# Performance work log

Hardware: AMD Instinct MI355X
Metric: run time of the kernel (lower is better)

Reference implementation:

```python
import jax, jax.numpy as jnp
import numpy as np

INPUT_DIM = 128
HIDDEN = 64
NUM_LAYERS = 2
BATCH = 1024
SEQ = 512


def setup_inputs() -> dict:
    key = jax.random.key(0)
    ks = jax.random.split(key, 1 + 4 * NUM_LAYERS + 2)
    inp = {"x": jax.random.normal(ks[0], (BATCH, SEQ, INPUT_DIM), dtype=jnp.float32)}
    # PyTorch LSTM params per layer: W_ih [4H, in], W_hh [4H, H], b_ih [4H], b_hh [4H]
    # gate order: i, f, g, o. Init scale ~ 1/sqrt(H) like PyTorch uniform init.
    s = 1.0 / np.sqrt(HIDDEN)
    ki = 1
    for l in range(NUM_LAYERS):
        in_dim = INPUT_DIM if l == 0 else HIDDEN
        inp[f"W_ih{l}"] = jax.random.uniform(ks[ki], (4 * HIDDEN, in_dim), jnp.float32, -s, s); ki += 1
        inp[f"W_hh{l}"] = jax.random.uniform(ks[ki], (4 * HIDDEN, HIDDEN), jnp.float32, -s, s); ki += 1
        inp[f"b_ih{l}"] = jax.random.uniform(ks[ki], (4 * HIDDEN,), jnp.float32, -s, s); ki += 1
        inp[f"b_hh{l}"] = jax.random.uniform(ks[ki], (4 * HIDDEN,), jnp.float32, -s, s); ki += 1
    inp["fc_w"] = jax.random.uniform(ks[ki], (1, HIDDEN), jnp.float32, -s, s); ki += 1
    inp["fc_b"] = jax.random.uniform(ks[ki], (1,), jnp.float32, -s, s)
    return inp


def _lstm_layer(x, W_ih, W_hh, b_ih, b_hh):
    # x: [B, T, in] -> h_seq: [B, T, H]
    B, T, _ = x.shape
    H = W_hh.shape[1]
    # Precompute input contribution for all timesteps (the big GEMM).
    xg = jnp.einsum('bti,gi->btg', x, W_ih) + b_ih + b_hh  # [B, T, 4H]

    def step(carry, xg_t):
        h, c = carry
        g = xg_t + h @ W_hh.T  # [B, 4H]
        i, f, gg, o = jnp.split(g, 4, axis=-1)
        i = jax.nn.sigmoid(i)
        f = jax.nn.sigmoid(f)
        gg = jnp.tanh(gg)
        o = jax.nn.sigmoid(o)
        c = f * c + i * gg
        h = o * jnp.tanh(c)
        return (h, c), h

    init = (jnp.zeros((B, H), x.dtype), jnp.zeros((B, H), x.dtype))
    _, hs = jax.lax.scan(step, init, jnp.swapaxes(xg, 0, 1))  # hs: [T, B, H]
    return jnp.swapaxes(hs, 0, 1)


def reference(x, W_ih0, W_hh0, b_ih0, b_hh0, W_ih1, W_hh1, b_ih1, b_hh1, fc_w, fc_b):
    h = _lstm_layer(x, W_ih0, W_hh0, b_ih0, b_hh0)
    h = _lstm_layer(h, W_ih1, W_hh1, b_ih1, b_hh1)  # dropout inactive at inference
    last = h[:, -1, :]  # [B, H]
    return jax.nn.sigmoid(last @ fc_w.T + fc_b)  # [B, 1]
```

## Files before the change

kernel.cpp:

```cpp
#include <hip/hip_runtime.h>
#include <hip/hip_bf16.h>

using short8  = __attribute__((ext_vector_type(8))) short;
using float4v = __attribute__((ext_vector_type(4))) float;
using uint2v  = __attribute__((ext_vector_type(2))) unsigned int;
using u32 = unsigned int;
using u16 = unsigned short;

#define MFMA(a,b,cc) __builtin_amdgcn_mfma_f32_16x16x32_bf16((a),(b),(cc),0,0,0)
#define PIPE_BARRIER() asm volatile("s_waitcnt lgkmcnt(0)\n\ts_barrier" ::: "memory")
#define LOG2E 1.44269504088896340736f

static __device__ __forceinline__ float fexp2(float x){ return __builtin_amdgcn_exp2f(x); }
static __device__ __forceinline__ float frcp(float x){ return __builtin_amdgcn_rcpf(x); }

static __device__ __forceinline__ short f2bf(float f){
  __hip_bfloat16 h = __float2bfloat16(f);
  return __builtin_bit_cast(short, h);
}
static __device__ __forceinline__ short8 load_bf8s(const float* p, float s){
  short8 v;
#pragma unroll
  for (int j = 0; j < 8; ++j) v[j] = f2bf(p[j] * s);
  return v;
}
static __device__ __forceinline__ float bflo(u32 d){ return __builtin_bit_cast(float, d << 16); }
static __device__ __forceinline__ float bfhi(u32 d){ return __builtin_bit_cast(float, d & 0xffff0000u); }

static __device__ __forceinline__ float gates1(float ai, float af, float ag, float ao, float& cst){
  float iv = frcp(1.f + fexp2(ai));
  float fv = frcp(1.f + fexp2(af));
  float ov = frcp(1.f + fexp2(ao));
  float gv = 1.f - 2.f * frcp(1.f + fexp2(ag));
  float cn = fv * cst + iv * gv;
  cst = cn;
  float tc = 1.f - 2.f * frcp(1.f + fexp2((2.f*LOG2E) * cn));
  return ov * tc;
}

template<int KK>
static __device__ __forceinline__ void gm4_part(int t0, const float* xlane,
    float4v (&xr)[4][2], float4v (&acc)[4], const short8 (&wA)[4][4])
{
  short8 xb;
#pragma unroll
  for (int j = 0; j < 4; ++j){ xb[j] = f2bf(xr[KK][0][j]); xb[4+j] = f2bf(xr[KK][1][j]); }
  int tn = t0 + 4; if (tn > 508) tn = 508;
  const float* nx = xlane + (size_t)tn * 128 + KK*32;
  xr[KK][0] = *(const float4v*)nx;
  xr[KK][1] = *(const float4v*)(nx + 4);
  acc[0] = MFMA(xb, wA[0][KK], acc[0]);
  acc[1] = MFMA(xb, wA[1][KK], acc[1]);
  acc[2] = MFMA(xb, wA[2][KK], acc[2]);
  acc[3] = MFMA(xb, wA[3][KK], acc[3]);
}

static __device__ __forceinline__ void gm4_store(int t0,
    float4v (&acc)[4], u32 (&xgb)[8][4][132], int c, int kg, int wl)
{
  u32* base = &xgb[(t0 + kg) & 7][0][(wl*16 + c)*2];
#pragma unroll
  for (int r = 0; r < 4; ++r){
    u32 d0 = (u32)(u16)f2bf(acc[0][r]) | ((u32)(u16)f2bf(acc[1][r]) << 16);
    u32 d1 = (u32)(u16)f2bf(acc[2][r]) | ((u32)(u16)f2bf(acc[3][r]) << 16);
    uint2v dv = {d0, d1};
    *(uint2v*)(base + r*132) = dv;
  }
#pragma unroll
  for (int gt = 0; gt < 4; ++gt) acc[gt] = (float4v){0.f,0.f,0.f,0.f};
}

template<int P>
static __device__ __forceinline__ void l0_step(int slot,
    const u32 (&xgb)[8][4][132],
    const short8 (&wA)[4][4], const float (&bs)[4],
    float& cst, __hip_bfloat16 (&h0s)[2][16][72],
    float (*tp)[20], int lane, int c, int kg, int wl)
{
  short8 hf0 = *(const short8*)&h0s[P^1][c][kg*8];
  short8 hf1 = *(const short8*)&h0s[P^1][c][32 + kg*8];
  uint2v xgd = *(const uint2v*)&xgb[slot][kg][(wl*16 + c)*2];
  float4v av[4];
#pragma unroll
  for (int gt = 0; gt < 4; ++gt) av[gt] = (float4v){0.f,0.f,0.f,0.f};
  av[0] = MFMA(hf0, wA[0][0], av[0]); av[1] = MFMA(hf0, wA[1][0], av[1]);
  av[2] = MFMA(hf0, wA[2][0], av[2]); av[3] = MFMA(hf0, wA[3][0], av[3]);
  av[0] = MFMA(hf1, wA[0][1], av[0]); av[1] = MFMA(hf1, wA[1][1], av[1]);
  av[2] = MFMA(hf1, wA[2][1], av[2]); av[3] = MFMA(hf1, wA[3][1], av[3]);
  if (lane < 16){
#pragma unroll
    for (int r = 0; r < 4; ++r){
      float4v t_ = {av[0][r], av[1][r], av[2][r], av[3][r]};
      *(float4v*)&tp[lane][r*4] = t_;
    }
  }
  float4v g4 = *(const float4v*)&tp[c][kg*4];
  float ai = g4[0] + bs[0] + bflo(xgd[0]);
  float af = g4[1] + bs[1] + bfhi(xgd[0]);
  float ag = g4[2] + bs[2] + bflo(xgd[1]);
  float ao = g4[3] + bs[3] + bfhi(xgd[1]);
  float hv = gates1(ai, af, ag, ao, cst);
  h0s[P][kg][wl*16 + c] = __float2bfloat16(hv);
}

template<int TPAR>
static __device__ __forceinline__ void l1_step(bool last,
    const short8 (&wA)[4][4], const float (&bs)[4],
    float& cst,
    const __hip_bfloat16 (&h0s)[2][16][72], __hip_bfloat16 (&h1s)[2][16][72],
    float (*tp)[20], float (*hfin)[64], int lane, int c, int kg, int wl)
{
  short8 a0 = *(const short8*)&h0s[TPAR][c][kg*8];
  short8 a1 = *(const short8*)&h0s[TPAR][c][32 + kg*8];
  short8 b0 = *(const short8*)&h1s[TPAR^1][c][kg*8];
  short8 b1 = *(const short8*)&h1s[TPAR^1][c][32 + kg*8];
  float4v av[4];
#pragma unroll
  for (int gt = 0; gt < 4; ++gt) av[gt] = (float4v){0.f,0.f,0.f,0.f};
  av[0] = MFMA(a0, wA[0][0], av[0]); av[1] = MFMA(a0, wA[1][0], av[1]);
  av[2] = MFMA(a0, wA[2][0], av[2]); av[3] = MFMA(a0, wA[3][0], av[3]);
  av[0] = MFMA(a1, wA[0][1], av[0]); av[1] = MFMA(a1, wA[1][1], av[1]);
  av[2] = MFMA(a1, wA[2][1], av[2]); av[3] = MFMA(a1, wA[3][1], av[3]);
  av[0] = MFMA(b0, wA[0][2], av[0]); av[1] = MFMA(b0, wA[1][2], av[1]);
  av[2] = MFMA(b0, wA[2][2], av[2]); av[3] = MFMA(b0, wA[3][2], av[3]);
  av[0] = MFMA(b1, wA[0][3], av[0]); av[1] = MFMA(b1, wA[1][3], av[1]);
  av[2] = MFMA(b1, wA[2][3], av[2]); av[3] = MFMA(b1, wA[3][3], av[3]);
  if (lane < 16){
#pragma unroll
    for (int r = 0; r < 4; ++r){
      float4v t_ = {av[0][r], av[1][r], av[2][r], av[3][r]};
      *(float4v*)&tp[lane][r*4] = t_;
    }
  }
  float4v g4 = *(const float4v*)&tp[c][kg*4];
  float hv = gates1(g4[0]+bs[0], g4[1]+bs[1], g4[2]+bs[2], g4[3]+bs[3], cst);
  h1s[TPAR][kg][wl*16 + c] = __float2bfloat16(hv);
  if (last) hfin[kg][wl*16 + c] = hv;
}

__global__ __attribute__((amdgpu_flat_work_group_size(768, 768), amdgpu_waves_per_eu(3, 3)))
void lstm_fused(
    const float* __restrict__ x,
    const float* __restrict__ Wih0, const float* __restrict__ Whh0,
    const float* __restrict__ bih0, const float* __restrict__ bhh0,
    const float* __restrict__ Wih1, const float* __restrict__ Whh1,
    const float* __restrict__ bih1, const float* __restrict__ bhh1,
    const float* __restrict__ fcw,  const float* __restrict__ fcb,
    float* __restrict__ out)
{
  constexpr int T = 512;
  const int tid  = threadIdx.x;
  const int lane = tid & 63;
  const int wv   = tid >> 6;
  const int grp  = wv >> 2;
  const int wl   = wv & 3;
  const int c    = lane & 15;
  const int kg   = lane >> 4;
  const int bblk = blockIdx.x;

  __shared__ __align__(16) __hip_bfloat16 h0s[2][16][72];
  __shared__ __align__(16) __hip_bfloat16 h1s[2][16][72];
  __shared__ __align__(16) u32  xgb[8][4][132];
  __shared__ __align__(16) float tmp[2][4][16][20];
  __shared__ float hfin[4][64];

  {
    __hip_bfloat16 z = __float2bfloat16(0.f);
    for (int i = tid; i < 2*16*72; i += 768){
      (&h0s[0][0][0])[i] = z;
      (&h1s[0][0][0])[i] = z;
    }
  }

  const float gsc[4] = {-LOG2E, -LOG2E, 2.f*LOG2E, -LOG2E};

  short8 wA[4][4];
  float  bs[4] = {0.f, 0.f, 0.f, 0.f};
  const int urow = wl*16 + c;
  if (grp == 0){
#pragma unroll
    for (int gt = 0; gt < 4; ++gt){
      const int row = gt*64 + urow;
#pragma unroll
      for (int kk = 0; kk < 2; ++kk){
        wA[gt][kk]   = load_bf8s(Whh0 + row*64 + kk*32 + kg*8, gsc[gt]);
        wA[gt][kk+2] = wA[gt][kk];
      }
      bs[gt] = (bih0[row] + bhh0[row]) * gsc[gt];
    }
  } else if (grp == 1){
#pragma unroll
    for (int gt = 0; gt < 4; ++gt){
      const int row = gt*64 + urow;
#pragma unroll
      for (int kk = 0; kk < 2; ++kk){
        wA[gt][kk]   = load_bf8s(Wih1 + row*64 + kk*32 + kg*8, gsc[gt]);
        wA[gt][kk+2] = load_bf8s(Whh1 + row*64 + kk*32 + kg*8, gsc[gt]);
      }
      bs[gt] = (bih1[row] + bhh1[row]) * gsc[gt];
    }
  } else {
#pragma unroll
    for (int gt = 0; gt < 4; ++gt){
      const int row = gt*64 + urow;
#pragma unroll
      for (int kk = 0; kk < 4; ++kk)
        wA[gt][kk] = load_bf8s(Wih0 + row*128 + kk*32 + kg*8, gsc[gt]);
    }
  }

  const float* xlane = nullptr;
  float4v xr[4][2];
  float4v acc[4];
#pragma unroll
  for (int gt = 0; gt < 4; ++gt) acc[gt] = (float4v){0.f,0.f,0.f,0.f};
  if (grp == 2){
    xlane = x + (size_t)(bblk*4 + (c & 3)) * T * 128 + (c >> 2)*128 + kg*8;
#pragma unroll
    for (int kk = 0; kk < 4; ++kk){
      xr[kk][0] = *(const float4v*)(xlane + kk*32);
      xr[kk][1] = *(const float4v*)(xlane + kk*32 + 4);
    }
  }
  float cst = 0.f;
  float (*tp)[20] = tmp[grp & 1][wl];

  __syncthreads();

  if (grp == 2){
    gm4_part<0>(0, xlane, xr, acc, wA);
    gm4_part<1>(0, xlane, xr, acc, wA);
    gm4_part<2>(0, xlane, xr, acc, wA);
    gm4_part<3>(0, xlane, xr, acc, wA);
    gm4_store(0, acc, xgb, c, kg, wl);
  }
  PIPE_BARRIER();

  for (int lt = 0; lt < T; lt += 4){
    const int sb = lt & 7;
    const int t0 = lt + 4;
    const bool prod = (lt <= 504);
    if (grp == 0) l0_step<0>(sb+0, xgb, wA, bs, cst, h0s, tp, lane, c, kg, wl);
    else if (grp == 1){ if (lt > 0) l1_step<1>(false, wA, bs, cst, h0s, h1s, tp, hfin, lane, c, kg, wl); }
    else if (prod) gm4_part<0>(t0, xlane, xr, acc, wA);
    PIPE_BARRIER();
    if (grp == 0) l0_step<1>(sb+1, xgb, wA, bs, cst, h0s, tp, lane, c, kg, wl);
    else if (grp == 1) l1_step<0>(false, wA, bs, cst, h0s, h1s, tp, hfin, lane, c, kg, wl);
    else if (prod) gm4_part<1>(t0, xlane, xr, acc, wA);
    PIPE_BARRIER();
    if (grp == 0) l0_step<0>(sb+2, xgb, wA, bs, cst, h0s, tp, lane, c, kg, wl);
    else if (grp == 1) l1_step<1>(false, wA, bs, cst, h0s, h1s, tp, hfin, lane, c, kg, wl);
    else if (prod) gm4_part<2>(t0, xlane, xr, acc, wA);
    PIPE_BARRIER();
    if (grp == 0) l0_step<1>(sb+3, xgb, wA, bs, cst, h0s, tp, lane, c, kg, wl);
    else if (grp == 1) l1_step<0>(false, wA, bs, cst, h0s, h1s, tp, hfin, lane, c, kg, wl);
    else if (prod){ gm4_part<3>(t0, xlane, xr, acc, wA); gm4_store(t0, acc, xgb, c, kg, wl); }
    PIPE_BARRIER();
  }
  if (grp == 1)
    l1_step<1>(true, wA, bs, cst, h0s, h1s, tp, hfin, lane, c, kg, wl);
  __syncthreads();

  if (tid < 4){
    float s = fcb[0];
#pragma unroll
    for (int k = 0; k < 64; ++k) s += hfin[tid][k] * fcw[k];
    out[bblk*4 + tid] = frcp(1.f + fexp2(-LOG2E * s));
  }
}

extern "C" void kernel_launch(void* const* d_in, const int* in_sizes, int n_in,
                              void* d_out, int out_size, void* d_ws, size_t ws_size,
                              hipStream_t stream) {
  const float* x    = (const float*)d_in[0];
  const float* Wih0 = (const float*)d_in[1];
  const float* Whh0 = (const float*)d_in[2];
  const float* bih0 = (const float*)d_in[3];
  const float* bhh0 = (const float*)d_in[4];
  const float* Wih1 = (const float*)d_in[5];
  const float* Whh1 = (const float*)d_in[6];
  const float* bih1 = (const float*)d_in[7];
  const float* bhh1 = (const float*)d_in[8];
  const float* fcw  = (const float*)d_in[9];
  const float* fcb  = (const float*)d_in[10];
  float* out = (float*)d_out;

  hipLaunchKernelGGL(lstm_fused, dim3(256), dim3(768), 0, stream,
                     x, Wih0, Whh0, bih0, bhh0, Wih1, Whh1, bih1, bhh1,
                     fcw, fcb, out);
}
```

Before: 345.0 us.

## Replace workgroup barriers with LDS progress-counter spin synchronization between wave groups

Removes the per-step s_barrier that locked the layer-0, layer-1 and input-GEMM wave groups into one shared schedule. Each wave now publishes a progress counter in LDS and spins only on the counters it depends on, so the groups can drift relative to each other within the ring-buffer slack. This is meant to cut barrier stalls on the recurrent critical path. In exchange it adds LDS polling traffic, and it depends on LDS memory ordering and the waitcnt placement for correctness, so races or hangs are possible.

```diff
diff --git a/kernel.cpp b/kernel.cpp
--- a/kernel.cpp
+++ b/kernel.cpp
@@ -8,7 +8,7 @@
 using u16 = unsigned short;
 
 #define MFMA(a,b,cc) __builtin_amdgcn_mfma_f32_16x16x32_bf16((a),(b),(cc),0,0,0)
-#define PIPE_BARRIER() asm volatile("s_waitcnt lgkmcnt(0)\n\ts_barrier" ::: "memory")
+#define LGKM0() asm volatile("s_waitcnt lgkmcnt(0)" ::: "memory")
 #define LOG2E 1.44269504088896340736f
 
 static __device__ __forceinline__ float fexp2(float x){ return __builtin_amdgcn_exp2f(x); }
@@ -38,6 +38,23 @@
   return ov * tc;
 }
 
+static __device__ __forceinline__ int spin4(volatile int* p, int v){
+  int m;
+  for(;;){
+    int a = p[0], b = p[1], c2 = p[2], d = p[3];
+    m = min(min(a,b), min(c2,d));
+    if (m >= v) break;
+  }
+  asm volatile("" ::: "memory");
+  return m;
+}
+static __device__ __forceinline__ int spin1(volatile int* p, int v){
+  int a;
+  for(;;){ a = *p; if (a >= v) break; }
+  asm volatile("" ::: "memory");
+  return a;
+}
+
 template<int KK>
 static __device__ __forceinline__ void gm4_part(int t0, const float* xlane,
     float4v (&xr)[4][2], float4v (&acc)[4], const short8 (&wA)[4][4])
@@ -70,16 +87,15 @@
   for (int gt = 0; gt < 4; ++gt) acc[gt] = (float4v){0.f,0.f,0.f,0.f};
 }
 
-template<int P>
-static __device__ __forceinline__ void l0_step(int slot,
-    const u32 (&xgb)[8][4][132],
-    const short8 (&wA)[4][4], const float (&bs)[4],
-    float& cst, __hip_bfloat16 (&h0s)[2][16][72],
-    float (*tp)[20], int lane, int c, int kg, int wl)
-{
+static __device__ __forceinline__ void l0_body(int t,
+    const u32 (&xgb)[8][4][132], const short8 (&wA)[4][4], const float (&bs)[4],
+    float& cst, __hip_bfloat16 (&h0s)[2][16][72], float (*tp)[20],
+    int lane, int c, int kg, int wl)
+{
+  const int P = t & 1, RS = t & 7;
   short8 hf0 = *(const short8*)&h0s[P^1][c][kg*8];
   short8 hf1 = *(const short8*)&h0s[P^1][c][32 + kg*8];
-  uint2v xgd = *(const uint2v*)&xgb[slot][kg][(wl*16 + c)*2];
+  uint2v xgd = *(const uint2v*)&xgb[RS][kg][(wl*16 + c)*2];
   float4v av[4];
 #pragma unroll
   for (int gt = 0; gt < 4; ++gt) av[gt] = (float4v){0.f,0.f,0.f,0.f};
@@ -103,17 +119,17 @@
   h0s[P][kg][wl*16 + c] = __float2bfloat16(hv);
 }
 
-template<int TPAR>
-static __device__ __forceinline__ void l1_step(bool last,
+static __device__ __forceinline__ void l1_body(int s,
     const short8 (&wA)[4][4], const float (&bs)[4],
     float& cst,
     const __hip_bfloat16 (&h0s)[2][16][72], __hip_bfloat16 (&h1s)[2][16][72],
     float (*tp)[20], float (*hfin)[64], int lane, int c, int kg, int wl)
 {
-  short8 a0 = *(const short8*)&h0s[TPAR][c][kg*8];
-  short8 a1 = *(const short8*)&h0s[TPAR][c][32 + kg*8];
-  short8 b0 = *(const short8*)&h1s[TPAR^1][c][kg*8];
-  short8 b1 = *(const short8*)&h1s[TPAR^1][c][32 + kg*8];
+  const int TP = s & 1;
+  short8 a0 = *(const short8*)&h0s[TP][c][kg*8];
+  short8 a1 = *(const short8*)&h0s[TP][c][32 + kg*8];
+  short8 b0 = *(const short8*)&h1s[TP^1][c][kg*8];
+  short8 b1 = *(const short8*)&h1s[TP^1][c][32 + kg*8];
   float4v av[4];
 #pragma unroll
   for (int gt = 0; gt < 4; ++gt) av[gt] = (float4v){0.f,0.f,0.f,0.f};
@@ -134,8 +150,8 @@
   }
   float4v g4 = *(const float4v*)&tp[c][kg*4];
   float hv = gates1(g4[0]+bs[0], g4[1]+bs[1], g4[2]+bs[2], g4[3]+bs[3], cst);
-  h1s[TPAR][kg][wl*16 + c] = __float2bfloat16(hv);
-  if (last) hfin[kg][wl*16 + c] = hv;
+  h1s[TP][kg][wl*16 + c] = __float2bfloat16(hv);
+  if (s == 511) hfin[kg][wl*16 + c] = hv;
 }
 
 __global__ __attribute__((amdgpu_flat_work_group_size(768, 768), amdgpu_waves_per_eu(3, 3)))
@@ -162,6 +178,7 @@
   __shared__ __align__(16) __hip_bfloat16 h1s[2][16][72];
   __shared__ __align__(16) u32  xgb[8][4][132];
   __shared__ __align__(16) float tmp[2][4][16][20];
+  __shared__ __align__(16) int  prog[3][4];
   __shared__ float hfin[4][64];
 
   {
@@ -170,6 +187,7 @@
       (&h0s[0][0][0])[i] = z;
       (&h1s[0][0][0])[i] = z;
     }
+    if (tid < 12) ((int*)prog)[tid] = 0;
   }
 
   const float gsc[4] = {-LOG2E, -LOG2E, 2.f*LOG2E, -LOG2E};
@@ -227,38 +245,41 @@
 
   __syncthreads();
 
-  if (grp == 2){
-    gm4_part<0>(0, xlane, xr, acc, wA);
-    gm4_part<1>(0, xlane, xr, acc, wA);
-    gm4_part<2>(0, xlane, xr, acc, wA);
-    gm4_part<3>(0, xlane, xr, acc, wA);
-    gm4_store(0, acc, xgb, c, kg, wl);
-  }
-  PIPE_BARRIER();
-
-  for (int lt = 0; lt < T; lt += 4){
-    const int sb = lt & 7;
-    const int t0 = lt + 4;
-    const bool prod = (lt <= 504);
-    if (grp == 0) l0_step<0>(sb+0, xgb, wA, bs, cst, h0s, tp, lane, c, kg, wl);
-    else if (grp == 1){ if (lt > 0) l1_step<1>(false, wA, bs, cst, h0s, h1s, tp, hfin, lane, c, kg, wl); }
-    else if (prod) gm4_part<0>(t0, xlane, xr, acc, wA);
-    PIPE_BARRIER();
-    if (grp == 0) l0_step<1>(sb+1, xgb, wA, bs, cst, h0s, tp, lane, c, kg, wl);
-    else if (grp == 1) l1_step<0>(false, wA, bs, cst, h0s, h1s, tp, hfin, lane, c, kg, wl);
-    else if (prod) gm4_part<1>(t0, xlane, xr, acc, wA);
-    PIPE_BARRIER();
-    if (grp == 0) l0_step<0>(sb+2, xgb, wA, bs, cst, h0s, tp, lane, c, kg, wl);
-    else if (grp == 1) l1_step<1>(false, wA, bs, cst, h0s, h1s, tp, hfin, lane, c, kg, wl);
-    else if (prod) gm4_part<2>(t0, xlane, xr, acc, wA);
-    PIPE_BARRIER();
-    if (grp == 0) l0_step<1>(sb+3, xgb, wA, bs, cst, h0s, tp, lane, c, kg, wl);
-    else if (grp == 1) l1_step<0>(false, wA, bs, cst, h0s, h1s, tp, hfin, lane, c, kg, wl);
-    else if (prod){ gm4_part<3>(t0, xlane, xr, acc, wA); gm4_store(t0, acc, xgb, c, kg, wl); }
-    PIPE_BARRIER();
-  }
-  if (grp == 1)
-    l1_step<1>(true, wA, bs, cst, h0s, h1s, tp, hfin, lane, c, kg, wl);
+  if (grp == 0){
+    int gseen = 0, l0seen = 0, l1seen = 0;
+    volatile int* gp = &prog[2][wl];
+    for (int t = 0; t < T; ++t){
+      if (gseen < t + 1)              gseen  = spin1(gp, t + 1);
+      if (l0seen < t)                 l0seen = spin4(prog[0], t);
+      if (t >= 2 && l1seen < t - 1)   l1seen = spin4(prog[1], t - 1);
+      l0_body(t, xgb, wA, bs, cst, h0s, tp, lane, c, kg, wl);
+      LGKM0();
+      *(volatile int*)&prog[0][wl] = t + 1;
+    }
+  } else if (grp == 1){
+    int l0seen = 0, l1seen = 0;
+    for (int s = 0; s < T; ++s){
+      if (l0seen < s + 1)  l0seen = spin4(prog[0], s + 1);
+      if (l1seen < s)      l1seen = spin4(prog[1], s);
+      l1_body(s, wA, bs, cst, h0s, h1s, tp, hfin, lane, c, kg, wl);
+      LGKM0();
+      *(volatile int*)&prog[1][wl] = s + 1;
+    }
+  } else {
+    int l0seen = 0;
+    volatile int* lp = &prog[0][wl];
+    for (int t0 = 0; t0 < T; t0 += 4){
+      gm4_part<0>(t0, xlane, xr, acc, wA);
+      gm4_part<1>(t0, xlane, xr, acc, wA);
+      gm4_part<2>(t0, xlane, xr, acc, wA);
+      gm4_part<3>(t0, xlane, xr, acc, wA);
+      if (t0 >= 8 && l0seen < t0 - 4) l0seen = spin1(lp, t0 - 4);
+      gm4_store(t0, acc, xgb, c, kg, wl);
+      LGKM0();
+      *(volatile int*)&prog[2][wl] = t0 + 4;
+    }
+  }
+
   __syncthreads();
 
   if (tid < 4){
```

Result: slower. 441.9 us (+28.1%).
